# Optimization experiments

Measured on AMD Instinct MI355X. Metric: run time of the kernel, lower is better.

The kernel has to match this reference:

```python
import jax, jax.numpy as jnp
import numpy as np

VOCAB = 50000
WORD_EMB = 300
N_QNODE = 3
N_KNODE = 3
HID = 512
N_OUT = 300
N_ANS = 32000
N_LAYERS = 3
MIN_NORM = 1e-15
EPS = 1e-7

# ---- Hyperboloid manifold ops (HGCN convention, curvature c, K = 1/c) ----

def proj_tan0(u):
    # zero out the time coordinate
    return u.at[..., :1].set(0.0)

def expmap0(u, c):
    K = 1.0 / c
    sqrtK = jnp.sqrt(K)
    d = u[..., 1:]
    n = jnp.clip(jnp.linalg.norm(d, axis=-1, keepdims=True), MIN_NORM, None)
    theta = n / sqrtK
    return jnp.concatenate([sqrtK * jnp.cosh(theta), sqrtK * jnp.sinh(theta) * d / n], axis=-1)

def logmap0(x, c):
    K = 1.0 / c
    sqrtK = jnp.sqrt(K)
    d = x[..., 1:]
    n = jnp.clip(jnp.linalg.norm(d, axis=-1, keepdims=True), MIN_NORM, None)
    theta = jnp.clip(x[..., :1] / sqrtK, 1.0 + EPS, None)
    rest = sqrtK * jnp.arccosh(theta) * d / n
    return jnp.concatenate([jnp.zeros_like(rest[..., :1]), rest], axis=-1)

def proj(x, c):
    K = 1.0 / c
    d = x[..., 1:]
    first = jnp.sqrt(jnp.clip(K + jnp.sum(d * d, axis=-1, keepdims=True), EPS, None))
    return jnp.concatenate([first, d], axis=-1)

def hyperbolic_emb(x, c):
    return proj(expmap0(proj_tan0(x), c), c)


def setup_inputs() -> dict:
    key = jax.random.key(0)
    ks = jax.random.split(key, 16)
    B, NQ, NK = 256, 30, 100
    inp = {}
    inp['he_ques_id'] = jax.random.randint(ks[0], (B, NQ, N_QNODE), 0, VOCAB)
    inp['he_kg_id'] = jax.random.randint(ks[1], (B, NK, N_KNODE), 0, VOCAB)
    inp['emb_table'] = jax.random.normal(ks[2], (VOCAB, WORD_EMB), jnp.float32)
    inp['q2h_w'] = jax.random.normal(ks[3], (WORD_EMB * N_QNODE, HID), jnp.float32) * 0.01
    inp['q2h_b'] = jnp.zeros((HID,), jnp.float32)
    inp['k2h_w'] = jax.random.normal(ks[4], (WORD_EMB * N_KNODE, HID), jnp.float32) * 0.01
    inp['k2h_b'] = jnp.zeros((HID,), jnp.float32)
    inp['Wk'] = jax.random.normal(ks[5], (N_LAYERS, HID, HID), jnp.float32) * 0.05
    inp['Wq'] = jax.random.normal(ks[6], (N_LAYERS, HID, HID), jnp.float32) * 0.05
    inp['curv'] = jnp.ones((N_LAYERS + 1,), jnp.float32)
    inp['proj1_w'] = jax.random.normal(ks[7], (2 * HID, HID), jnp.float32) * 0.02
    inp['proj1_b'] = jnp.zeros((HID,), jnp.float32)
    inp['proj2_w'] = jax.random.normal(ks[8], (HID, N_OUT), jnp.float32) * 0.02
    inp['proj2_b'] = jnp.zeros((N_OUT,), jnp.float32)
    inp['glove_cands'] = jax.random.normal(ks[9], (N_ANS, N_OUT), jnp.float32)
    return inp


def reference(he_ques_id, he_kg_id, emb_table, q2h_w, q2h_b, k2h_w, k2h_b,
              Wk, Wq, curv, proj1_w, proj1_b, proj2_w, proj2_b, glove_cands):
    B = he_ques_id.shape[0]
    c0 = curv[0]
    cL = curv[N_LAYERS]

    # embedding lookup + flatten hyperedge nodes
    he_q = emb_table[he_ques_id].reshape(B, he_ques_id.shape[1], -1)  # (B,Nq,900)
    he_k = emb_table[he_kg_id].reshape(B, he_kg_id.shape[1], -1)      # (B,Nk,900)
    he_q = jnp.where(jnp.isnan(he_q), 0.0, he_q)
    he_k = jnp.where(jnp.isnan(he_k), 0.0, he_k)

    he_q = he_q @ q2h_w + q2h_b   # (B,Nq,H)
    he_k = he_k @ k2h_w + k2h_b   # (B,Nk,H)

    q = hyperbolic_emb(he_q, c0)  # (B,Nq,H) on hyperboloid
    k = hyperbolic_emb(he_k, c0)  # (B,Nk,H)

    scale = 1.0 / np.sqrt(HID)
    for i in range(N_LAYERS):
        c_in, c_out = curv[i], curv[i + 1]
        kt = proj_tan0(logmap0(k, c_in))
        qt = proj_tan0(logmap0(q, c_in))
        kp = kt @ Wk[i]
        qp = qt @ Wq[i]
        s = jnp.einsum('bkh,bqh->bkq', kp, qp) * scale
        att_k = jnp.einsum('bkq,bqh->bkh', jax.nn.softmax(s, axis=-1), qt) + kt
        att_q = jnp.einsum('bqk,bkh->bqh', jax.nn.softmax(jnp.swapaxes(s, 1, 2), axis=-1), kt) + qt
        k = proj(expmap0(proj_tan0(att_k), c_out), c_out)
        q = proj(expmap0(proj_tan0(att_q), c_out), c_out)

    # mean pool over hyperedges, concat kg||ques
    last_kq = jnp.concatenate([k.mean(axis=1), q.mean(axis=1)], axis=1)  # (B,2H)
    euc = proj_tan0(logmap0(last_kq, cL))
    h = jax.nn.relu(euc @ proj1_w + proj1_b)
    out = h @ proj2_w + proj2_b               # (B,300)
    sim = out @ glove_cands.T                 # (B,32000)
    pred = jax.nn.log_softmax(sim, axis=1)
    return pred
```

## Files before the change

kernel.cpp:

```cpp
#include <hip/hip_runtime.h>
#include <math.h>

#define BATCH 256
#define NQ 30
#define NK 100
#define HID 512
#define WORD 300
#define KIN 900
#define KP 928
#define NANS 32000
#define NOUT 300
#define NOUTP 384
#define NTG 12
#define NLAYERS 3
#define MQT (BATCH * NQ)
#define MKT (BATCH * NK)
#define SCALE 0.044194173824159216f
#define KTLD 520
#define CLDST 136
#define SST 36
#define PQLD 136

typedef __attribute__((ext_vector_type(8))) short bf16x8;
typedef __attribute__((ext_vector_type(4))) float f32x4;
typedef unsigned short ushort_t;

__device__ __forceinline__ unsigned short f2bf(float f) {
  unsigned int u = __float_as_uint(f);
  u = (u + 0x7FFF + ((u >> 16) & 1)) >> 16;
  return (unsigned short)u;
}
__device__ __forceinline__ float bf2f(unsigned short s) {
  return __uint_as_float(((unsigned int)s) << 16);
}

typedef const __attribute__((address_space(1))) unsigned int* gas_u32;
typedef __attribute__((address_space(3))) unsigned int* las_u32;
__device__ __forceinline__ void gld_lds16(const void* g, void* l) {
  __builtin_amdgcn_global_load_lds((gas_u32)g, (las_u32)l, 16, 0, 0);
}

__device__ __forceinline__ int xcd_swz_linear() {
  const int nwg = gridDim.x * gridDim.y;
  const int orig = blockIdx.y * gridDim.x + blockIdx.x;
  const int q = nwg >> 3, r = nwg & 7;
  const int xcd = orig & 7, idx = orig >> 3;
  return (xcd < r ? xcd * (q + 1) : r * (q + 1) + (xcd - r) * q) + idx;
}

__device__ __forceinline__ float waveReduceSum(float v) {
#pragma unroll
  for (int o = 32; o > 0; o >>= 1) v += __shfl_xor(v, o);
  return v;
}
__device__ float blockReduceSum512(float v) {
  __shared__ float sm[8];
  int lane = threadIdx.x & 63, w = threadIdx.x >> 6;
  v = waveReduceSum(v);
  if (lane == 0) sm[w] = v;
  __syncthreads();
  float r = 0.f;
#pragma unroll
  for (int i = 0; i < 8; ++i) r += sm[i];
  __syncthreads();
  return r;
}

template <int SWZB, int BIAS, int OUTF32, int OUTBF16, int ZC0, int RELU>
__global__ __launch_bounds__(256) void mfma_gemm2(
    const ushort_t* __restrict__ A1, const ushort_t* __restrict__ Bt1,
    const float* __restrict__ bias1, float* __restrict__ C1,
    ushort_t* __restrict__ Cb1, int M1b,
    const ushort_t* __restrict__ A2, const ushort_t* __restrict__ Bt2,
    const float* __restrict__ bias2, float* __restrict__ C2,
    ushort_t* __restrict__ Cb2,
    size_t zsA, size_t zsB, size_t zsC,
    int N, int K, int nbias) {
  __shared__ __align__(16) ushort_t smem[128 * CLDST];
  const int wg = xcd_swz_linear();
  const int bx = wg % gridDim.x, by = wg / gridDim.x;
  const int z = blockIdx.z;
  const bool sel = (by >= M1b);
  const ushort_t* A = (sel ? A2 : A1) + z * zsA;
  const ushort_t* Bt = (sel ? Bt2 : Bt1) + z * zsB;
  const float* bias = sel ? bias2 : bias1;
  float* C = (sel ? C2 : C1);
  ushort_t* Cb = (sel ? Cb2 : Cb1);
  if (C) C += z * zsC;
  if (Cb) Cb += z * zsC;
  const int row0 = (sel ? (by - M1b) : by) * 128;
  const int col0 = bx * 128;

  const int tid = threadIdx.x;
  const int lane = tid & 63, w = tid >> 6;
  const int wr = w >> 1, wc = w & 1;
  const int s_r = lane & 15, s_kq = lane >> 4;
  const int nt = K / 32;

  const size_t a_src0 = (size_t)(row0 + (w * 2 + 0) * 16 + s_r) * K + s_kq * 8;
  const size_t a_src1 = (size_t)(row0 + (w * 2 + 1) * 16 + s_r) * K + s_kq * 8;
  const size_t b_lin0 = (size_t)(col0 + (w * 2 + 0) * 16 + s_r) * K + s_kq * 8;
  const size_t b_lin1 = (size_t)(col0 + (w * 2 + 1) * 16 + s_r) * K + s_kq * 8;
  const size_t b_swz0 = ((size_t)(col0 >> 7) * nt) * 4096 + (w * 2 + 0) * 512 + lane * 8;
  const size_t b_swz1 = b_swz0 + 512;

  auto stageAB = [&](int t, int bsel) {
    const int k0 = t * 32;
    ushort_t* Ab = smem + bsel * 4096;
    ushort_t* Bb = smem + 8192 + bsel * 4096;
    gld_lds16(A + a_src0 + k0, Ab + (w * 2 + 0) * 512);
    gld_lds16(A + a_src1 + k0, Ab + (w * 2 + 1) * 512);
    if (SWZB) {
      gld_lds16(Bt + b_swz0 + (size_t)t * 4096, Bb + (w * 2 + 0) * 512);
      gld_lds16(Bt + b_swz1 + (size_t)t * 4096, Bb + (w * 2 + 1) * 512);
    } else {
      gld_lds16(Bt + b_lin0 + k0, Bb + (w * 2 + 0) * 512);
      gld_lds16(Bt + b_lin1 + k0, Bb + (w * 2 + 1) * 512);
    }
  };

  f32x4 acc[4][4];
#pragma unroll
  for (int i = 0; i < 4; ++i)
#pragma unroll
    for (int j = 0; j < 4; ++j) acc[i][j] = (f32x4){0.f, 0.f, 0.f, 0.f};

  stageAB(0, 0);
  __syncthreads();
  for (int t = 0; t < nt; ++t) {
    const int cur = t & 1;
    if (t + 1 < nt) stageAB(t + 1, cur ^ 1);
    const ushort_t* Ab = smem + cur * 4096;
    const ushort_t* Bb = smem + 8192 + cur * 4096;
    bf16x8 af[4], bfr[4];
#pragma unroll
    for (int mi = 0; mi < 4; ++mi)
      af[mi] = *(const bf16x8*)(Ab + (wr * 4 + mi) * 512 + lane * 8);
#pragma unroll
    for (int nj = 0; nj < 4; ++nj)
      bfr[nj] = *(const bf16x8*)(Bb + (wc * 4 + nj) * 512 + lane * 8);
#pragma unroll
    for (int mi = 0; mi < 4; ++mi)
#pragma unroll
      for (int nj = 0; nj < 4; ++nj)
        acc[mi][nj] = __builtin_amdgcn_mfma_f32_16x16x32_bf16(
            af[mi], bfr[nj], acc[mi][nj], 0, 0, 0);
    __syncthreads();
  }

  if (OUTBF16) {
#pragma unroll
    for (int nj = 0; nj < 4; ++nj) {
      const int nl = wc * 64 + nj * 16 + (lane & 15);
      const int n = col0 + nl;
      const float bb = BIAS ? ((n < nbias) ? bias[n] : 0.f) : 0.f;
#pragma unroll
      for (int mi = 0; mi < 4; ++mi) {
        f32x4 v = acc[mi][nj];
#pragma unroll
        for (int r = 0; r < 4; ++r) {
          const int ml = wr * 64 + mi * 16 + (lane >> 4) * 4 + r;
          float val = v[r] + bb;
          if (RELU) val = fmaxf(val, 0.f);
          if (ZC0 && n == 0) val = 0.f;
          smem[ml * CLDST + nl] = f2bf(val);
        }
      }
    }
    __syncthreads();
#pragma unroll
    for (int j = 0; j < 8; ++j) {
      const int e = j * 2048 + tid * 8;
      const int ml = e >> 7, nl = e & 127;
      uint4 v = *(const uint4*)(smem + ml * CLDST + nl);
      *(uint4*)(Cb + (size_t)(row0 + ml) * N + col0 + nl) = v;
    }
  }
  if (OUTF32) {
#pragma unroll
    for (int nj = 0; nj < 4; ++nj) {
      const int n = col0 + wc * 64 + nj * 16 + (lane & 15);
      const float bb = BIAS ? ((n < nbias) ? bias[n] : 0.f) : 0.f;
#pragma unroll
      for (int mi = 0; mi < 4; ++mi) {
        f32x4 v = acc[mi][nj];
#pragma unroll
        for (int r = 0; r < 4; ++r) {
          const int m = row0 + wr * 64 + mi * 16 + (lane >> 4) * 4 + r;
          float val = v[r] + bb;
          if (RELU) val = fmaxf(val, 0.f);
          if (ZC0 && n == 0) val = 0.f;
          C[(size_t)m * N + n] = val;
        }
      }
    }
  }
}

__global__ __launch_bounds__(256) void gather_all_k(
    const int* __restrict__ qid, const int* __restrict__ kid,
    const float* __restrict__ emb, ushort_t* __restrict__ gq,
    ushort_t* __restrict__ gk) {
  int m = blockIdx.x;
  const int* ids;
  ushort_t* outp;
  if (m < MQT) {
    ids = qid + m * 3;
    outp = gq + (size_t)m * KP;
  } else {
    m -= MQT;
    ids = kid + m * 3;
    outp = gk + (size_t)m * KP;
  }
  const int t = threadIdx.x;
  if (t >= KP / 4) return;
  const int k = t * 4;
  ushort4 o = make_ushort4(0, 0, 0, 0);
  if (k < KIN) {
    const int node = (k >= 600) ? 2 : ((k >= 300) ? 1 : 0);
    const int off = k - node * 300;
    const int id = ids[node];
    float4 v = *(const float4*)(emb + (size_t)id * 300 + off);
    if (v.x != v.x) v.x = 0.f;
    if (v.y != v.y) v.y = 0.f;
    if (v.z != v.z) v.z = 0.f;
    if (v.w != v.w) v.w = 0.f;
    o = make_ushort4(f2bf(v.x), f2bf(v.y), f2bf(v.z), f2bf(v.w));
  }
  *(ushort4*)(outp + k) = o;
}

__global__ __launch_bounds__(256) void tcast4_k(
    const float* __restrict__ q2h_w, const float* __restrict__ k2h_w,
    const float* __restrict__ p1w, const float* __restrict__ p2w,
    ushort_t* __restrict__ q2h_wt, ushort_t* __restrict__ k2h_wt,
    ushort_t* __restrict__ p1wt, ushort_t* __restrict__ p2wt) {
  const int z = blockIdx.z;
  const float* src;
  ushort_t* dst;
  int R, Cc, Rp, Cp;
  if (z == 0)      { src = q2h_w; dst = q2h_wt; R = KIN;  Cc = HID;  Rp = KP;   Cp = HID; }
  else if (z == 1) { src = k2h_w; dst = k2h_wt; R = KIN;  Cc = HID;  Rp = KP;   Cp = HID; }
  else if (z == 2) { src = p1w; dst = p1wt; R = 1024; Cc = HID;  Rp = 1024; Cp = HID; }
  else             { src = p2w; dst = p2wt; R = HID;  Cc = NOUT; Rp = HID;  Cp = NOUTP; }
  const int r0 = blockIdx.y * 32, c0 = blockIdx.x * 32;
  if (r0 >= Rp || c0 >= Cp) return;
  __shared__ float t[32][33];
  const int tx = threadIdx.x & 31, ty = threadIdx.x >> 5;
#pragma unroll
  for (int i = 0; i < 4; ++i) {
    int r = r0 + ty + i * 8, c = c0 + tx;
    t[ty + i * 8][tx] = (r < R && c < Cc) ? src[(size_t)r * Cc + c] : 0.f;
  }
  __syncthreads();
#pragma unroll
  for (int i = 0; i < 4; ++i) {
    int c = c0 + ty + i * 8, r = r0 + tx;
    if (c < Cp && r < Rp) dst[(size_t)c * Rp + r] = f2bf(t[tx][ty + i * 8]);
  }
}

__global__ __launch_bounds__(256) void gcast_swz_k(
    const float* __restrict__ glove, ushort_t* __restrict__ gs) {
  const int ts = blockIdx.x, gp = blockIdx.y;
  ushort_t* dst = gs + ((size_t)gp * NTG + ts) * 4096;
  for (int g = threadIdx.x; g < 512; g += 256) {
    const int o = g * 8;
    const int chunk = o >> 9, kq = (o >> 7) & 3, rl = (o >> 3) & 15;
    const int row = gp * 128 + chunk * 16 + rl;
    const int kb = ts * 32 + kq * 8;
    ushort_t tmp[8];
    if (kb + 8 <= NOUT) {
      const float* s = glove + (size_t)row * NOUT + kb;
      float2 a0 = *(const float2*)(s + 0);
      float2 a1 = *(const float2*)(s + 2);
      float2 a2 = *(const float2*)(s + 4);
      float2 a3 = *(const float2*)(s + 6);
      tmp[0] = f2bf(a0.x); tmp[1] = f2bf(a0.y);
      tmp[2] = f2bf(a1.x); tmp[3] = f2bf(a1.y);
      tmp[4] = f2bf(a2.x); tmp[5] = f2bf(a2.y);
      tmp[6] = f2bf(a3.x); tmp[7] = f2bf(a3.y);
    } else {
#pragma unroll
      for (int j = 0; j < 8; ++j) {
        const int k = kb + j;
        tmp[j] = (k < NOUT) ? f2bf(glove[(size_t)row * NOUT + k]) : (ushort_t)0;
      }
    }
    *(ushort4*)(dst + o) = make_ushort4(tmp[0], tmp[1], tmp[2], tmp[3]);
    *(ushort4*)(dst + o + 4) = make_ushort4(tmp[4], tmp[5], tmp[6], tmp[7]);
  }
}

__global__ __launch_bounds__(128) void castrows_k(
    const float* __restrict__ Wk, const float* __restrict__ Wq,
    ushort_t* __restrict__ Wkr, ushort_t* __restrict__ Wqr) {
  const int idx = blockIdx.x;
  const int mat = idx >> 9, row = idx & 511;
  const float* src = (mat < 3 ? Wk + (size_t)mat * HID * HID
                              : Wq + (size_t)(mat - 3) * HID * HID) + (size_t)row * HID;
  ushort_t* dst = (mat < 3 ? Wkr + (size_t)mat * HID * HID
                           : Wqr + (size_t)(mat - 3) * HID * HID) + (size_t)row * HID;
  const int k = threadIdx.x * 4;
  float4 v = *(const float4*)(src + k);
  *(ushort4*)(dst + k) = make_ushort4(f2bf(v.x), f2bf(v.y), f2bf(v.z), f2bf(v.w));
}

__global__ __launch_bounds__(512) void att_fused_k(
    const ushort_t* __restrict__ Qp, const ushort_t* __restrict__ Ktc,
    const ushort_t* __restrict__ Qc, ushort_t* __restrict__ Kn,
    ushort_t* __restrict__ Qn) {
  const int b = blockIdx.x;
  __shared__ __align__(16) float S_lds[112 * SST];
  __shared__ __align__(16) ushort_t Pq[32 * PQLD];
  __shared__ __align__(16) ushort_t kts[NK * KTLD];
  __shared__ __align__(16) ushort_t qts[NQ * HID];
  const int tid = threadIdx.x;
  const int w = tid >> 6, lane = tid & 63;
  const ushort_t* ktg = Ktc + (size_t)b * NK * HID;
  const ushort_t* qtg = Qc + (size_t)b * NQ * HID;

  for (int e = tid; e < NK * 64; e += 512) {
    const int r = e >> 6, c16 = e & 63;
    gld_lds16(ktg + (size_t)r * HID + c16 * 8, kts + (size_t)r * KTLD + c16 * 8);
  }
  for (int e = tid; e < NQ * 64; e += 512) {
    const int r = e >> 6, c16 = e & 63;
    gld_lds16(qtg + (size_t)r * HID + c16 * 8, qts + (size_t)r * HID + c16 * 8);
  }
  __syncthreads();

  if (w < 7) {
    const int r = lane & 15, kq = lane >> 4;
    const ushort_t* qpb = Qp + (size_t)b * NQ * HID;
    const int rowA = w * 16 + r;
    const int rowA_c = (rowA < NK) ? rowA : (NK - 1);
    const int qr1 = (16 + r) < NQ ? (16 + r) : NQ - 1;
    f32x4 a0 = {0.f, 0.f, 0.f, 0.f}, a1 = {0.f, 0.f, 0.f, 0.f};
    for (int k0 = 0; k0 < HID; k0 += 32) {
      bf16x8 af = *(const bf16x8*)(kts + (size_t)rowA_c * KTLD + k0 + kq * 8);
      bf16x8 b0 = *(const bf16x8*)(qpb + (size_t)r * HID + k0 + kq * 8);
      bf16x8 b1 = *(const bf16x8*)(qpb + (size_t)qr1 * HID + k0 + kq * 8);
      a0 = __builtin_amdgcn_mfma_f32_16x16x32_bf16(af, b0, a0, 0, 0, 0);
      a1 = __builtin_amdgcn_mfma_f32_16x16x32_bf16(af, b1, a1, 0, 0, 0);
    }
    const int q0 = lane & 15, mb = (lane >> 4) * 4;
#pragma unroll
    for (int rr = 0; rr < 4; ++rr) {
      const int mA = w * 16 + mb + rr;
      if (mA < NK) {
        S_lds[mA * SST + q0] = a0[rr] * SCALE;
        if (q0 + 16 < NQ) S_lds[mA * SST + q0 + 16] = a1[rr] * SCALE;
      }
    }
  }
  __syncthreads();
  float e2[NQ];
  float inv2 = 0.f;
  const int kr2 = tid - 32;
  const bool do2b = (kr2 >= 0 && kr2 < NK);
  if (tid < NQ) {
    const int q = tid;
    float m = -1e30f;
    for (int kr = 0; kr < NK; ++kr) m = fmaxf(m, S_lds[kr * SST + q]);
    float s = 0.f;
    for (int kr = 0; kr < NK; ++kr) s += expf(S_lds[kr * SST + q] - m);
    float inv = 1.f / s;
    for (int kr = 0; kr < NK; ++kr)
      Pq[q * PQLD + kr] = f2bf(expf(S_lds[kr * SST + q] - m) * inv);
    for (int kr = NK; kr < 128; ++kr) Pq[q * PQLD + kr] = 0;
  } else if (tid < 32) {
    for (int kr = 0; kr < 128; ++kr) Pq[tid * PQLD + kr] = 0;
  } else if (do2b) {
    float m = -1e30f;
#pragma unroll
    for (int q = 0; q < NQ; ++q) m = fmaxf(m, S_lds[kr2 * SST + q]);
    float s = 0.f;
#pragma unroll
    for (int q = 0; q < NQ; ++q) {
      e2[q] = expf(S_lds[kr2 * SST + q] - m);
      s += e2[q];
    }
    inv2 = 1.f / s;
  }
  __syncthreads();
  ushort_t* Pk = (ushort_t*)S_lds;
  if (do2b) {
    ushort_t* prow = Pk + kr2 * 72;
#pragma unroll
    for (int q = 0; q < NQ; ++q) prow[q] = f2bf(e2[q] * inv2);
    prow[30] = 0;
    prow[31] = 0;
  }
  __syncthreads();

  const int cl = lane & 15, g8 = (lane >> 4) * 8;
  {
    bf16x8 bk[4];
#pragma unroll
    for (int nt = 0; nt < 4; ++nt) {
      const int col = w * 64 + nt * 16 + cl;
      union { ushort_t u[8]; bf16x8 v; } pb;
#pragma unroll
      for (int j = 0; j < 8; ++j) {
        const int q = g8 + j;
        pb.u[j] = qts[(q < NQ ? q : NQ - 1) * HID + col];
      }
      bk[nt] = pb.v;
    }
    ushort_t* kout = Kn + (size_t)b * NK * HID;
#pragma unroll
    for (int mt = 0; mt < 7; ++mt) {
      bf16x8 af = *(const bf16x8*)(Pk + (mt * 16 + cl) * 72 + g8);
      f32x4 ac[4];
#pragma unroll
      for (int nt = 0; nt < 4; ++nt) {
        ac[nt] = (f32x4){0.f, 0.f, 0.f, 0.f};
        ac[nt] = __builtin_amdgcn_mfma_f32_16x16x32_bf16(af, bk[nt], ac[nt], 0, 0, 0);
      }
#pragma unroll
      for (int nt = 0; nt < 4; ++nt) {
        const int col = w * 64 + nt * 16 + cl;
#pragma unroll
        for (int r = 0; r < 4; ++r) {
          const int row = mt * 16 + (lane >> 4) * 4 + r;
          if (row < NK) {
            float v = ac[nt][r] + bf2f(kts[(size_t)row * KTLD + col]);
            kout[(size_t)row * HID + col] = f2bf(v);
          }
        }
      }
    }
  }
  {
    f32x4 aq[2][4];
#pragma unroll
    for (int mt = 0; mt < 2; ++mt)
#pragma unroll
      for (int nt = 0; nt < 4; ++nt) aq[mt][nt] = (f32x4){0.f, 0.f, 0.f, 0.f};
#pragma unroll
    for (int ks = 0; ks < 4; ++ks) {
      bf16x8 bq[4];
#pragma unroll
      for (int nt = 0; nt < 4; ++nt) {
        const int col = w * 64 + nt * 16 + cl;
        union { ushort_t u[8]; bf16x8 v; } pb;
#pragma unroll
        for (int j = 0; j < 8; ++j) {
          const int kr = ks * 32 + g8 + j;
          pb.u[j] = kts[(size_t)(kr < NK ? kr : NK - 1) * KTLD + col];
        }
        bq[nt] = pb.v;
      }
#pragma unroll
      for (int mt = 0; mt < 2; ++mt) {
        bf16x8 af = *(const bf16x8*)(Pq + (mt * 16 + cl) * PQLD + ks * 32 + g8);
#pragma unroll
        for (int nt = 0; nt < 4; ++nt)
          aq[mt][nt] = __builtin_amdgcn_mfma_f32_16x16x32_bf16(af, bq[nt], aq[mt][nt], 0, 0, 0);
      }
    }
    ushort_t* qout = Qn + (size_t)b * NQ * HID;
#pragma unroll
    for (int mt = 0; mt < 2; ++mt)
#pragma unroll
      for (int nt = 0; nt < 4; ++nt) {
        const int col = w * 64 + nt * 16 + cl;
#pragma unroll
        for (int r = 0; r < 4; ++r) {
          const int row = mt * 16 + (lane >> 4) * 4 + r;
          if (row < NQ) {
            float v = aq[mt][nt][r] + bf2f(qts[(size_t)row * HID + col]);
            qout[(size_t)row * HID + col] = f2bf(v);
          }
        }
      }
  }
}

__global__ __launch_bounds__(512) void finale_k(
    const ushort_t* __restrict__ Kb, const ushort_t* __restrict__ Qb,
    ushort_t* __restrict__ lastb, const float* __restrict__ curv) {
  const int b = blockIdx.x, tid = threadIdx.x;
  const int w = tid >> 6, lane = tid & 63;
  const float c = curv[NLAYERS];
  const float Kc = 1.f / c, sqrtK = sqrtf(Kc);
  __shared__ float fsc[NK + NQ];
  __shared__ float fst[NK + NQ];
  const ushort_t* xkp = Kb + (size_t)b * NK * HID;
  const ushort_t* xqp = Qb + (size_t)b * NQ * HID;

  for (int r = w; r < NK + NQ; r += 8) {
    const ushort_t* row =
        (r < NK) ? (xkp + (size_t)r * HID) : (xqp + (size_t)(r - NK) * HID);
    bf16x8 v = *(const bf16x8*)(row + lane * 8);
    float ss = 0.f;
#pragma unroll
    for (int j = 0; j < 8; ++j) {
      float t = bf2f((unsigned short)v[j]);
      ss = fmaf(t, t, ss);
    }
    ss = waveReduceSum(ss);
    if (lane == 0) {
      float n = fmaxf(sqrtf(ss), 1e-15f);
      float f = sqrtK * sinhf(n / sqrtK) / n;
      fsc[r] = f;
      fst[r] = sqrtf(fmaxf(Kc + f * f * ss, 1e-7f));
    }
  }
  __syncthreads();

  float mk, mq;
  if (tid == 0) {
    float sk = 0.f, sq2 = 0.f;
    for (int r = 0; r < NK; ++r) sk += fst[r];
    for (int r = 0; r < NQ; ++r) sq2 += fst[NK + r];
    mk = sk;
    mq = sq2;
  } else {
    float sk = 0.f, sq2 = 0.f;
    for (int r = 0; r < NK; ++r)
      sk = fmaf(fsc[r], bf2f(xkp[(size_t)r * HID + tid]), sk);
    for (int r = 0; r < NQ; ++r)
      sq2 = fmaf(fsc[NK + r], bf2f(xqp[(size_t)r * HID + tid]), sq2);
    mk = sk;
    mq = sq2;
  }
  mk *= (1.f / NK);
  mq *= (1.f / NQ);

  float sq = ((tid == 0) ? 0.f : mk * mk) + mq * mq;
  float ssall = blockReduceSum512(sq);
  __shared__ float x0sh;
  if (tid == 0) x0sh = mk;
  __syncthreads();
  const float x0 = x0sh;
  const float n = fmaxf(sqrtf(ssall), 1e-15f);
  const float theta = fmaxf(x0 / sqrtK, 1.f + 1e-7f);
  const float rr = sqrtK * acoshf(theta) / n;
  ushort_t* ob = lastb + (size_t)b * 1024;
  ob[tid] = (tid == 0) ? (ushort_t)0 : f2bf(rr * mk);
  ob[512 + tid] = f2bf(rr * mq);
}

__global__ __launch_bounds__(512) void logsoftmax_k(float* __restrict__ x) {
  const int b = blockIdx.x, tid = threadIdx.x;
  float4* row = (float4*)(x + (size_t)b * NANS);
  float m = -3.4e38f, s = 0.f;
  for (int i = tid; i < NANS / 4; i += 512) {
    float4 v = row[i];
    float lm = fmaxf(fmaxf(v.x, v.y), fmaxf(v.z, v.w));
    float nm = fmaxf(m, lm);
    s = s * expf(m - nm) + expf(v.x - nm) + expf(v.y - nm) +
        expf(v.z - nm) + expf(v.w - nm);
    m = nm;
  }
#pragma unroll
  for (int o = 32; o > 0; o >>= 1) {
    float mo = __shfl_xor(m, o);
    float so = __shfl_xor(s, o);
    float nm = fmaxf(m, mo);
    s = s * expf(m - nm) + so * expf(mo - nm);
    m = nm;
  }
  __shared__ float smm[8], sms[8];
  const int w = tid >> 6, lane = tid & 63;
  if (lane == 0) { smm[w] = m; sms[w] = s; }
  __syncthreads();
  float gm = smm[0], gs = sms[0];
#pragma unroll
  for (int i = 1; i < 8; ++i) {
    float nm = fmaxf(gm, smm[i]);
    gs = gs * expf(gm - nm) + sms[i] * expf(smm[i] - nm);
    gm = nm;
  }
  const float lse = gm + logf(gs);
  for (int i = tid; i < NANS / 4; i += 512) {
    float4 v = row[i];
    v.x -= lse; v.y -= lse; v.z -= lse; v.w -= lse;
    row[i] = v;
  }
}

extern "C" void kernel_launch(void* const* d_in, const int* in_sizes, int n_in,
                              void* d_out, int out_size, void* d_ws, size_t ws_size,
                              hipStream_t stream) {
  const int* qid = (const int*)d_in[0];
  const int* kid = (const int*)d_in[1];
  const float* emb = (const float*)d_in[2];
  const float* q2h_w = (const float*)d_in[3];
  const float* q2h_b = (const float*)d_in[4];
  const float* k2h_w = (const float*)d_in[5];
  const float* k2h_b = (const float*)d_in[6];
  const float* Wk = (const float*)d_in[7];
  const float* Wq = (const float*)d_in[8];
  const float* curv = (const float*)d_in[9];
  const float* p1w = (const float*)d_in[10];
  const float* p1b = (const float*)d_in[11];
  const float* p2w = (const float*)d_in[12];
  const float* p2b = (const float*)d_in[13];
  const float* glove = (const float*)d_in[14];
  float* out = (float*)d_out;

  ushort_t* u = (ushort_t*)d_ws;
  ushort_t* Ks0 = u;
  ushort_t* Ks1 = Ks0 + (size_t)MKT * HID;
  ushort_t* Qs0 = Ks1 + (size_t)MKT * HID;
  ushort_t* Qs1 = Qs0 + (size_t)MQT * HID;
  ushort_t* Qps = Qs1 + (size_t)MQT * HID;
  ushort_t* gq = Qps + (size_t)MQT * HID;
  ushort_t* gk = gq + (size_t)MQT * KP;
  ushort_t* q2h_wt = gk + (size_t)MKT * KP;
  ushort_t* k2h_wt = q2h_wt + (size_t)HID * KP;
  ushort_t* Wkr = k2h_wt + (size_t)HID * KP;
  ushort_t* Wqr = Wkr + (size_t)NLAYERS * HID * HID;
  ushort_t* Mb = Wqr + (size_t)NLAYERS * HID * HID;
  ushort_t* p1wt = Mb + (size_t)NLAYERS * HID * HID;
  ushort_t* p2wt = p1wt + (size_t)HID * 1024;
  ushort_t* lastb = p2wt + (size_t)NOUTP * HID;
  ushort_t* h1b = lastb + (size_t)BATCH * 1024;
  ushort_t* o2b = h1b + (size_t)BATCH * HID;
  ushort_t* gsw = o2b + (size_t)BATCH * NOUTP;

  gather_all_k<<<MQT + MKT, 256, 0, stream>>>(qid, kid, emb, gq, gk);
  tcast4_k<<<dim3(16, 32, 4), 256, 0, stream>>>(
      q2h_w, k2h_w, p1w, p2w, q2h_wt, k2h_wt, p1wt, p2wt);
  castrows_k<<<6 * HID, 128, 0, stream>>>(Wk, Wq, Wkr, Wqr);
  gcast_swz_k<<<dim3(NTG, 250), 256, 0, stream>>>(glove, gsw);

  mfma_gemm2<0, 0, 0, 1, 0, 0><<<dim3(HID / 128, HID / 128, NLAYERS), 256, 0, stream>>>(
      Wkr, Wqr, nullptr, nullptr, Mb, HID / 128,
      Wkr, Wqr, nullptr, nullptr, Mb,
      (size_t)HID * HID, (size_t)HID * HID, (size_t)HID * HID, HID, HID, HID);

  mfma_gemm2<0, 1, 0, 1, 1, 0><<<dim3(HID / 128, MQT / 128 + MKT / 128), 256, 0, stream>>>(
      gq, q2h_wt, q2h_b, nullptr, Qs0, MQT / 128,
      gk, k2h_wt, k2h_b, nullptr, Ks0, 0, 0, 0, HID, KP, HID);

  ushort_t* Kc = Ks0;
  ushort_t* Kn = Ks1;
  ushort_t* Qc = Qs0;
  ushort_t* Qn = Qs1;
  for (int i = 0; i < NLAYERS; ++i) {
    mfma_gemm2<0, 0, 0, 1, 0, 0><<<dim3(HID / 128, MQT / 128), 256, 0, stream>>>(
        Qc, Mb + (size_t)i * HID * HID, nullptr, nullptr, Qps, MQT / 128,
        Qc, Mb + (size_t)i * HID * HID, nullptr, nullptr, Qps,
        0, 0, 0, HID, HID, HID);
    att_fused_k<<<BATCH, 512, 0, stream>>>(Qps, Kc, Qc, Kn, Qn);
    ushort_t* t1 = Kc; Kc = Kn; Kn = t1;
    ushort_t* t2 = Qc; Qc = Qn; Qn = t2;
  }

  finale_k<<<BATCH, 512, 0, stream>>>(Kc, Qc, lastb, curv);

  mfma_gemm2<0, 1, 0, 1, 0, 1><<<dim3(HID / 128, BATCH / 128), 256, 0, stream>>>(
      lastb, p1wt, p1b, nullptr, h1b, BATCH / 128,
      lastb, p1wt, p1b, nullptr, h1b, 0, 0, 0, HID, 1024, HID);
  mfma_gemm2<0, 1, 0, 1, 0, 0><<<dim3(NOUTP / 128, BATCH / 128), 256, 0, stream>>>(
      h1b, p2wt, p2b, nullptr, o2b, BATCH / 128,
      h1b, p2wt, p2b, nullptr, o2b, 0, 0, 0, NOUTP, HID, NOUT);
  mfma_gemm2<1, 0, 1, 0, 0, 0><<<dim3(NANS / 128, BATCH / 128), 256, 0, stream>>>(
      o2b, gsw, nullptr, out, nullptr, BATCH / 128,
      o2b, gsw, nullptr, out, nullptr, 0, 0, 0, NANS, NOUTP, NANS);
  logsoftmax_k<<<BATCH, 512, 0, stream>>>(out);
}
```

Measured before the change: 402.2 us.

## Split attention kernel across two column halves and drop K staging in LDS

The fused attention kernel now launches two blocks per batch element, each owning 256 of the 512 hidden columns. K-output and Q-output work are split between wave groups instead of every wave doing both. The full K tile is no longer staged in LDS and only half the Q tile is, which greatly reduces LDS per block and allows more blocks per CU. In exchange, each block recomputes the whole score matrix, and K is read straight from global memory, including strided 2-byte gathers for the Q-side operand.

```diff
diff --git a/kernel.cpp b/kernel.cpp
--- a/kernel.cpp
+++ b/kernel.cpp
@@ -16,10 +16,10 @@
 #define MQT (BATCH * NQ)
 #define MKT (BATCH * NK)
 #define SCALE 0.044194173824159216f
-#define KTLD 520
 #define CLDST 136
 #define SST 36
 #define PQLD 136
+#define QTS 256
 
 typedef __attribute__((ext_vector_type(8))) short bf16x8;
 typedef __attribute__((ext_vector_type(4))) float f32x4;
@@ -310,25 +310,20 @@
     const ushort_t* __restrict__ Qp, const ushort_t* __restrict__ Ktc,
     const ushort_t* __restrict__ Qc, ushort_t* __restrict__ Kn,
     ushort_t* __restrict__ Qn) {
-  const int b = blockIdx.x;
+  const int b = blockIdx.y;
+  const int c0 = blockIdx.x * 256;
   __shared__ __align__(16) float S_lds[112 * SST];
   __shared__ __align__(16) ushort_t Pq[32 * PQLD];
-  __shared__ __align__(16) ushort_t kts[NK * KTLD];
-  __shared__ __align__(16) ushort_t qts[NQ * HID];
+  __shared__ __align__(16) ushort_t qts[NQ * QTS];
   const int tid = threadIdx.x;
   const int w = tid >> 6, lane = tid & 63;
-  const ushort_t* ktg = Ktc + (size_t)b * NK * HID;
+  const ushort_t* ktb = Ktc + (size_t)b * NK * HID;
   const ushort_t* qtg = Qc + (size_t)b * NQ * HID;
 
-  for (int e = tid; e < NK * 64; e += 512) {
-    const int r = e >> 6, c16 = e & 63;
-    gld_lds16(ktg + (size_t)r * HID + c16 * 8, kts + (size_t)r * KTLD + c16 * 8);
-  }
-  for (int e = tid; e < NQ * 64; e += 512) {
-    const int r = e >> 6, c16 = e & 63;
-    gld_lds16(qtg + (size_t)r * HID + c16 * 8, qts + (size_t)r * HID + c16 * 8);
-  }
-  __syncthreads();
+  for (int e = tid; e < NQ * 32; e += 512) {
+    const int r = e >> 5, c16 = e & 31;
+    gld_lds16(qtg + (size_t)r * HID + c0 + c16 * 8, qts + r * QTS + c16 * 8);
+  }
 
   if (w < 7) {
     const int r = lane & 15, kq = lane >> 4;
@@ -338,7 +333,7 @@
     const int qr1 = (16 + r) < NQ ? (16 + r) : NQ - 1;
     f32x4 a0 = {0.f, 0.f, 0.f, 0.f}, a1 = {0.f, 0.f, 0.f, 0.f};
     for (int k0 = 0; k0 < HID; k0 += 32) {
-      bf16x8 af = *(const bf16x8*)(kts + (size_t)rowA_c * KTLD + k0 + kq * 8);
+      bf16x8 af = *(const bf16x8*)(ktb + (size_t)rowA_c * HID + k0 + kq * 8);
       bf16x8 b0 = *(const bf16x8*)(qpb + (size_t)r * HID + k0 + kq * 8);
       bf16x8 b1 = *(const bf16x8*)(qpb + (size_t)qr1 * HID + k0 + kq * 8);
       a0 = __builtin_amdgcn_mfma_f32_16x16x32_bf16(af, b0, a0, 0, 0, 0);
@@ -395,16 +390,16 @@
   __syncthreads();
 
   const int cl = lane & 15, g8 = (lane >> 4) * 8;
-  {
+  if (w < 4) {
     bf16x8 bk[4];
 #pragma unroll
     for (int nt = 0; nt < 4; ++nt) {
-      const int col = w * 64 + nt * 16 + cl;
+      const int coll = w * 64 + nt * 16 + cl;
       union { ushort_t u[8]; bf16x8 v; } pb;
 #pragma unroll
       for (int j = 0; j < 8; ++j) {
         const int q = g8 + j;
-        pb.u[j] = qts[(q < NQ ? q : NQ - 1) * HID + col];
+        pb.u[j] = qts[(q < NQ ? q : NQ - 1) * QTS + coll];
       }
       bk[nt] = pb.v;
     }
@@ -420,19 +415,19 @@
       }
 #pragma unroll
       for (int nt = 0; nt < 4; ++nt) {
-        const int col = w * 64 + nt * 16 + cl;
+        const int col = c0 + w * 64 + nt * 16 + cl;
 #pragma unroll
         for (int r = 0; r < 4; ++r) {
           const int row = mt * 16 + (lane >> 4) * 4 + r;
           if (row < NK) {
-            float v = ac[nt][r] + bf2f(kts[(size_t)row * KTLD + col]);
+            float v = ac[nt][r] + bf2f(ktb[(size_t)row * HID + col]);
             kout[(size_t)row * HID + col] = f2bf(v);
           }
         }
       }
     }
-  }
-  {
+  } else {
+    const int w4 = w - 4;
     f32x4 aq[2][4];
 #pragma unroll
     for (int mt = 0; mt < 2; ++mt)
@@ -443,12 +438,12 @@
       bf16x8 bq[4];
 #pragma unroll
       for (int nt = 0; nt < 4; ++nt) {
-        const int col = w * 64 + nt * 16 + cl;
+        const int col = c0 + w4 * 64 + nt * 16 + cl;
         union { ushort_t u[8]; bf16x8 v; } pb;
 #pragma unroll
         for (int j = 0; j < 8; ++j) {
           const int kr = ks * 32 + g8 + j;
-          pb.u[j] = kts[(size_t)(kr < NK ? kr : NK - 1) * KTLD + col];
+          pb.u[j] = ktb[(size_t)(kr < NK ? kr : NK - 1) * HID + col];
         }
         bq[nt] = pb.v;
       }
@@ -465,12 +460,13 @@
     for (int mt = 0; mt < 2; ++mt)
 #pragma unroll
       for (int nt = 0; nt < 4; ++nt) {
-        const int col = w * 64 + nt * 16 + cl;
+        const int coll = w4 * 64 + nt * 16 + cl;
+        const int col = c0 + coll;
 #pragma unroll
         for (int r = 0; r < 4; ++r) {
           const int row = mt * 16 + (lane >> 4) * 4 + r;
           if (row < NQ) {
-            float v = aq[mt][nt][r] + bf2f(qts[(size_t)row * HID + col]);
+            float v = aq[mt][nt][r] + bf2f(qts[row * QTS + coll]);
             qout[(size_t)row * HID + col] = f2bf(v);
           }
         }
@@ -646,7 +642,7 @@
         Qc, Mb + (size_t)i * HID * HID, nullptr, nullptr, Qps, MQT / 128,
         Qc, Mb + (size_t)i * HID * HID, nullptr, nullptr, Qps,
         0, 0, 0, HID, HID, HID);
-    att_fused_k<<<BATCH, 512, 0, stream>>>(Qps, Kc, Qc, Kn, Qn);
+    att_fused_k<<<dim3(2, BATCH), 512, 0, stream>>>(Qps, Kc, Qc, Kn, Qn);
     ushort_t* t1 = Kc; Kc = Kn; Kn = t1;
     ushort_t* t2 = Qc; Qc = Qn; Qn = t2;
   }
```

After: 417.0 us. +3.7%, slower.
